# Kernel tuning notes

Hardware: AMD Instinct MI355X
Metric: run time of the kernel (lower is better)

The kernel has to match this reference:

```python
import jax, jax.numpy as jnp
import numpy as np

EPS = 1e-5

def _lrelu(x):
    return jnp.where(x >= 0, x, 0.2 * x)

def _bn(x, g, b):
    # train-mode BatchNorm2d over (B, N, k) per channel (channel-last layout)
    m = x.mean((0, 1, 2), keepdims=True)
    v = x.var((0, 1, 2), keepdims=True)  # biased variance, as torch uses for normalization
    return (x - m) * jax.lax.rsqrt(v + EPS) * g + b

def _knn(pos, k):
    # pos: (B, 3, N); negative squared euclidean distance, top-k = k nearest (incl. self)
    inner = -2.0 * jnp.einsum('bcn,bcm->bnm', pos, pos)
    xx = jnp.sum(pos * pos, axis=1)  # (B, N)
    pd = -xx[:, :, None] - inner - xx[:, None, :]  # (B, N, N)
    return jax.lax.top_k(pd, k)[1]  # (B, N, k) int32

def _edge(xt, idx):
    # xt: (B, N, C), idx: (B, N, k) -> (B, N, k, 2C) = [neighbor - center, center]
    nb = jax.vmap(lambda f, i: f[i])(xt, idx)  # (B, N, k, C) gather
    ctr = jnp.broadcast_to(xt[:, :, None, :], nb.shape)
    return jnp.concatenate([nb - ctr, ctr], axis=-1)

def _conv_bn_lrelu(h, W, g, b):
    # 1x1 conv as einsum on channel-last (B, N, k, Cin) -> (B, N, k, Cout)
    return _lrelu(_bn(jnp.einsum('bnkc,oc->bnko', h, W), g, b))

def _forward(x, k, W1, g1, b1, W2, g2, b2, W3, g3, b3, W4, g4, b4, W5, g5, b5, W9a, b9a, W9b, b9b):
    xt = x.transpose(0, 2, 1)  # (B, N, 67)
    idx = _knn(x[:, -3:, :], k)  # knn on xyz coords (dim9=True)
    h = _conv_bn_lrelu(_edge(xt, idx), W1, g1, b1)
    h = _conv_bn_lrelu(h, W2, g2, b2)
    x1 = h.max(axis=2)  # (B, N, 64) max over k neighbors
    h = _conv_bn_lrelu(_edge(x1, idx), W3, g3, b3)
    h = _conv_bn_lrelu(h, W4, g4, b4)
    x2 = h.max(axis=2)
    x3 = _conv_bn_lrelu(_edge(x2, idx), W5, g5, b5).max(axis=2)
    f = jnp.concatenate([x1, x2, x3], axis=-1)  # (B, N, 192)
    h = jax.nn.relu(jnp.einsum('bnc,oc->bno', f, W9a) + b9a)
    out = jnp.einsum('bnc,oc->bno', h, W9b) + b9b  # (B, N, 16)
    return out.transpose(0, 2, 1)  # (B, 16, N) to match torch layout

def setup_inputs() -> dict:
    key = jax.random.key(0)
    ks = jax.random.split(key, 8)
    B, C, N, K = 1, 67, 8192, 20
    s = 0.1
    return {
        'x': jax.random.normal(ks[0], (B, C, N), jnp.float32),
        'k': K,
        'W1': jax.random.normal(ks[1], (64, 134), jnp.float32) * s,
        'g1': jnp.ones((64,), jnp.float32), 'b1': jnp.zeros((64,), jnp.float32),
        'W2': jax.random.normal(ks[2], (64, 64), jnp.float32) * s,
        'g2': jnp.ones((64,), jnp.float32), 'b2': jnp.zeros((64,), jnp.float32),
        'W3': jax.random.normal(ks[3], (64, 128), jnp.float32) * s,
        'g3': jnp.ones((64,), jnp.float32), 'b3': jnp.zeros((64,), jnp.float32),
        'W4': jax.random.normal(ks[4], (64, 64), jnp.float32) * s,
        'g4': jnp.ones((64,), jnp.float32), 'b4': jnp.zeros((64,), jnp.float32),
        'W5': jax.random.normal(ks[5], (64, 128), jnp.float32) * s,
        'g5': jnp.ones((64,), jnp.float32), 'b5': jnp.zeros((64,), jnp.float32),
        'W9a': jax.random.normal(ks[6], (128, 192), jnp.float32) * s,
        'b9a': jnp.zeros((128,), jnp.float32),
        'W9b': jax.random.normal(ks[7], (16, 128), jnp.float32) * s,
        'b9b': jnp.zeros((16,), jnp.float32),
    }

def reference(x, k, W1, g1, b1, W2, g2, b2, W3, g3, b3, W4, g4, b4, W5, g5, b5, W9a, b9a, W9b, b9b):
    return _forward(x, k, W1, g1, b1, W2, g2, b2, W3, g3, b3, W4, g4, b4, W5, g5, b5, W9a, b9a, W9b, b9b)
```

## Files before the change

### kernel.cpp

```cpp
#include <hip/hip_runtime.h>

#define NPTS 8192
#define KNN  20
#define NREP 64
#define THSUB 2048
#define FCAP 256

__device__ __forceinline__ float pair_dist4(float qx, float qy, float qz, float xxn, float4 c) {
    float dot = fmaf(qz, c.z, fmaf(qy, c.y, qx * c.x));
    return fmaf(2.f, dot, -xxn) - c.w;
}
__device__ __forceinline__ float self_sq(float dx, float dy, float dz) {
    return fmaf(dz, dz, fmaf(dy, dy, dx * dx));
}
__device__ __forceinline__ float lrelu(float v) { return (v >= 0.f) ? v : 0.2f * v; }

__device__ __forceinline__ void compute_affine(const float* __restrict__ gs,
                                               const float* __restrict__ g,
                                               const float* __restrict__ b,
                                               float* saff, int tid) {
    if (tid < 64) {
        float s = 0.f, ss = 0.f;
        for (int r = 0; r < NREP; ++r) { s += gs[r * 128 + tid]; ss += gs[r * 128 + 64 + tid]; }
        const float invM = 1.f / (float)(NPTS * KNN);
        float mean = s * invM;
        float var = ss * invM - mean * mean;
        float sc = g[tid] * rsqrtf(var + 1e-5f);
        saff[tid] = sc;
        saff[64 + tid] = b[tid] - mean * sc;
    }
}

__global__ __launch_bounds__(256) void prep_kernel(const float* __restrict__ x,
                                                   const float* __restrict__ W1,
                                                   const float* __restrict__ W3,
                                                   const float* __restrict__ W5,
                                                   const float* __restrict__ W9a,
                                                   const float* __restrict__ W9b,
                                                   float4* __restrict__ pk,
                                                   float* __restrict__ Wt1,
                                                   float* __restrict__ Wt3,
                                                   float* __restrict__ Wt5,
                                                   float* __restrict__ W9at,
                                                   float* __restrict__ W9bt,
                                                   float* __restrict__ gsAll) {
    int gid = blockIdx.x * 256 + threadIdx.x;
    if (gid < NPTS) {
        float dx = x[64 * NPTS + gid], dy = x[65 * NPTS + gid], dz = x[66 * NPTS + gid];
        pk[gid] = make_float4(dx, dy, dz, self_sq(dx, dy, dz));
        return;
    }
    gid -= NPTS;
    if (gid < 67 * 128) {
        int c = gid >> 7, o = gid & 127;
        Wt1[gid] = (o < 64) ? W1[o * 134 + c] : W1[(o - 64) * 134 + 67 + c];
        return;
    }
    gid -= 67 * 128;
    if (gid < 64 * 128) {
        int c = gid >> 7, o = gid & 127;
        Wt3[gid] = (o < 64) ? W3[o * 128 + c] : W3[(o - 64) * 128 + 64 + c];
        return;
    }
    gid -= 64 * 128;
    if (gid < 64 * 128) {
        int c = gid >> 7, o = gid & 127;
        Wt5[gid] = (o < 64) ? W5[o * 128 + c] : W5[(o - 64) * 128 + 64 + c];
        return;
    }
    gid -= 64 * 128;
    if (gid < 192 * 128) {
        int c = gid >> 7, j = gid & 127;
        W9at[gid] = W9a[j * 192 + c];
        return;
    }
    gid -= 192 * 128;
    if (gid < 128 * 16) {
        int c = gid >> 4, j = gid & 15;
        W9bt[gid] = W9b[j * 128 + c];
        return;
    }
    gid -= 128 * 16;
    if (gid < 5 * NREP * 128) gsAll[gid] = 0.f;
}

__global__ __launch_bounds__(256) void knn_theta_proj(const float4* __restrict__ pk,
                                                      float* __restrict__ theta,
                                                      const float* __restrict__ X,
                                                      const float* __restrict__ Wt1,
                                                      float* __restrict__ P) {
    __shared__ float4 cpt[THSUB];
    int tid = threadIdx.x;
    if (blockIdx.x >= 512) {
        int bb = blockIdx.x - 512;
        int o = tid & 127, h = tid >> 7;
        int n0 = bb * 8 + h * 4;
        float acc[4] = {0.f, 0.f, 0.f, 0.f};
        for (int c = 0; c < 67; ++c) {
            float w = Wt1[c * 128 + o];
#pragma unroll
            for (int i = 0; i < 4; ++i) acc[i] = fmaf(X[(n0 + i) + c * NPTS], w, acc[i]);
        }
#pragma unroll
        for (int i = 0; i < 4; ++i) P[(n0 + i) * 128 + o] = acc[i];
        return;
    }
    int wid = tid >> 6, lane = tid & 63;
    int qbase = blockIdx.x * 16 + wid * 4;
    for (int i = tid; i < THSUB; i += 256) cpt[i] = pk[i];
    float qx[4], qy[4], qz[4], xxn[4], mv[4];
#pragma unroll
    for (int qi = 0; qi < 4; ++qi) {
        float4 qp = pk[qbase + qi];
        qx[qi] = qp.x; qy[qi] = qp.y; qz[qi] = qp.z; xxn[qi] = qp.w;
        mv[qi] = -INFINITY;
    }
    __syncthreads();
    for (int t = 0; t < THSUB / 64; ++t) {
        float4 c = cpt[t * 64 + lane];
#pragma unroll
        for (int qi = 0; qi < 4; ++qi)
            mv[qi] = fmaxf(mv[qi], pair_dist4(qx[qi], qy[qi], qz[qi], xxn[qi], c));
    }
#pragma unroll 1
    for (int qi = 0; qi < 4; ++qi) {
        float sel = mv[qi];
        float th = -INFINITY;
        for (int r = 0; r < KNN; ++r) {
            float v = sel;
#pragma unroll
            for (int m = 32; m >= 1; m >>= 1) v = fmaxf(v, __shfl_xor(v, m));
            th = v;
            unsigned long long bm = __ballot(sel == v);
            if (lane == __ffsll(bm) - 1) sel = -INFINITY;
        }
        if (lane == 0) theta[qbase + qi] = th - 1e-3f;
    }
}

__global__ __launch_bounds__(256) void knn_fsel(const float4* __restrict__ pk,
                                                const float* __restrict__ theta,
                                                int* __restrict__ idx_out,
                                                const float* __restrict__ P,
                                                float* __restrict__ gs) {
    __shared__ float4 cpt[1024];
    __shared__ int bufi[4][FCAP];
    int tid = threadIdx.x, wid = tid >> 6, lane = tid & 63;
    int q = blockIdx.x * 4 + wid;
    float4 qp = pk[q];
    float th = theta[q];
    int wcnt = 0;
    unsigned long long below = (1ull << lane) - 1ull;

    for (int ch = 0; ch < 8; ++ch) {
        __syncthreads();
        for (int i = tid; i < 1024; i += 256) cpt[i] = pk[ch * 1024 + i];
        __syncthreads();
        for (int t = 0; t < 16; ++t) {
            int gi = ch * 1024 + t * 64 + lane;
            float4 c = cpt[t * 64 + lane];
            float d = pair_dist4(qp.x, qp.y, qp.z, qp.w, c);
            bool p = (d >= th);
            unsigned long long mk = __ballot(p);
            if (p) {
                int pos = wcnt + (int)__popcll(mk & below);
                if (pos < FCAP) bufi[wid][pos] = gi;
            }
            wcnt += (int)__popcll(mk);
        }
    }

    int mi_keep = 0;
    if (wcnt <= FCAP) {
        float sv[4]; int si[4];
#pragma unroll
        for (int r = 0; r < 4; ++r) {
            int j = r * 64 + lane;
            bool ok = j < wcnt;
            int sidx = ok ? bufi[wid][j] : 0;
            float dv = pair_dist4(qp.x, qp.y, qp.z, qp.w, pk[sidx]);
            sv[r] = ok ? dv : -INFINITY;
            si[r] = ok ? sidx : 0x7fffffff;
        }
        for (int r = 0; r < KNN; ++r) {
            float lv = -INFINITY; int li = 0x7fffffff; int ls = -1;
#pragma unroll
            for (int s3 = 0; s3 < 4; ++s3) {
                bool g = (sv[s3] > lv) || (sv[s3] == lv && si[s3] < li);
                if (g) { lv = sv[s3]; li = si[s3]; ls = s3; }
            }
            float wv = lv; int wi = li;
#pragma unroll
            for (int m = 32; m >= 1; m >>= 1) {
                float ov = __shfl_xor(wv, m); int oi = __shfl_xor(wi, m);
                if (ov > wv || (ov == wv && oi < wi)) { wv = ov; wi = oi; }
            }
            if (lv == wv && li == wi) {
#pragma unroll
                for (int s3 = 0; s3 < 4; ++s3)
                    if (s3 == ls) { sv[s3] = -INFINITY; si[s3] = 0x7fffffff; }
            }
            if (lane == 0) idx_out[q * KNN + r] = wi;
            if (lane == r) mi_keep = wi;
        }
    } else {
        float pv = INFINITY; int pi = -1;
        for (int r = 0; r < KNN; ++r) {
            float bv = -INFINITY; int bi = 0x7fffffff;
            for (int t = 0; t < NPTS / 64; ++t) {
                int i = t * 64 + lane;
                float d = pair_dist4(qp.x, qp.y, qp.z, qp.w, pk[i]);
                bool adm = (d < pv) || (d == pv && i > pi);
                if (adm && (d > bv || (d == bv && i < bi))) { bv = d; bi = i; }
            }
            float wv = bv; int wi = bi;
#pragma unroll
            for (int m = 32; m >= 1; m >>= 1) {
                float ov = __shfl_xor(wv, m); int oi = __shfl_xor(wi, m);
                if (ov > wv || (ov == wv && oi < wi)) { wv = ov; wi = oi; }
            }
            if (lane == 0) idx_out[q * KNN + r] = wi;
            if (lane == r) mi_keep = wi;
            pv = wv; pi = wi;
        }
    }
    float An = P[q * 128 + lane];
    float Bn = P[q * 128 + 64 + lane];
    float base = Bn - An;
    float sum = 0.f, ss = 0.f;
#pragma unroll
    for (int kk = 0; kk < KNN; ++kk) {
        int m = __shfl(mi_keep, kk);
        float z = P[(size_t)m * 128 + lane] + base;
        sum += z;
        ss = fmaf(z, z, ss);
    }
    float* gg = gs + (blockIdx.x & (NREP - 1)) * 128;
    atomicAdd(gg + lane, sum);
    atomicAdd(gg + 64 + lane, ss);
}

__global__ __launch_bounds__(256) void zsum_kernel(const float* __restrict__ P,
                                                   const int* __restrict__ idx,
                                                   float* __restrict__ gs) {
    int tid = threadIdx.x;
    int o = tid & 63;
    float sum = 0.f, sumsq = 0.f;
    int n0 = blockIdx.x * 4;
#pragma unroll
    for (int ni = 0; ni < 4; ++ni) {
        int n = n0 + ni;
        float An = P[n * 128 + o];
        float Bn = P[n * 128 + 64 + o];
        float base = Bn - An;
#pragma unroll
        for (int kk2 = 0; kk2 < 5; ++kk2) {
            int kk = (tid >> 6) + kk2 * 4;
            int m = idx[n * KNN + kk];
            float z = P[m * 128 + o] + base;
            sum += z;
            sumsq = fmaf(z, z, sumsq);
        }
    }
    __shared__ float s1[256], s2[256];
    s1[tid] = sum; s2[tid] = sumsq;
    __syncthreads();
    if (tid < 64) {
        float a = s1[tid] + s1[tid + 64] + s1[tid + 128] + s1[tid + 192];
        float b = s2[tid] + s2[tid + 64] + s2[tid + 128] + s2[tid + 192];
        float* g = gs + (blockIdx.x & (NREP - 1)) * 128;
        atomicAdd(g + tid, a);
        atomicAdd(g + 64 + tid, b);
    }
}

__global__ __launch_bounds__(256) void conv_gemm_kernel(const float* __restrict__ P,
                                                        const int* __restrict__ idx,
                                                        const float* __restrict__ gsIn,
                                                        const float* __restrict__ gIn,
                                                        const float* __restrict__ bIn,
                                                        const float* __restrict__ W,
                                                        float* __restrict__ gsOut,
                                                        float* __restrict__ Mx,
                                                        float* __restrict__ Mn) {
    __shared__ float As[80][68];
    __shared__ float Ws[64][68];
    __shared__ float saff[128];
    int tid = threadIdx.x;
    int r0 = blockIdx.x * 80;

    compute_affine(gsIn, gIn, bIn, saff, tid);
    for (int i2 = tid; i2 < 1024; i2 += 256) {
        int rr = i2 >> 4, c4 = (i2 & 15) * 4;
        *(float4*)&Ws[rr][c4] = *(const float4*)&W[rr * 64 + c4];
    }
    __syncthreads();

#pragma unroll 5
    for (int i2 = tid; i2 < 1280; i2 += 256) {
        int rr = i2 >> 4, c4 = (i2 & 15) * 4;
        int grow = r0 + rr;
        int n = grow / 20;
        int m = idx[grow];
        float4 zn = *(const float4*)&P[(size_t)m * 128 + c4];
        float4 an = *(const float4*)&P[(size_t)n * 128 + c4];
        float4 bn = *(const float4*)&P[(size_t)n * 128 + 64 + c4];
        float4 ov; float z;
        z = zn.x + (bn.x - an.x); ov.x = lrelu(fmaf(z, saff[c4 + 0], saff[64 + c4 + 0]));
        z = zn.y + (bn.y - an.y); ov.y = lrelu(fmaf(z, saff[c4 + 1], saff[64 + c4 + 1]));
        z = zn.z + (bn.z - an.z); ov.z = lrelu(fmaf(z, saff[c4 + 2], saff[64 + c4 + 2]));
        z = zn.w + (bn.w - an.w); ov.w = lrelu(fmaf(z, saff[c4 + 3], saff[64 + c4 + 3]));
        *(float4*)&As[rr][c4] = ov;
    }
    __syncthreads();

    int ty = tid >> 4, tx = tid & 15;
    float acc[5][4];
#pragma unroll
    for (int i = 0; i < 5; ++i)
#pragma unroll
        for (int j = 0; j < 4; ++j) acc[i][j] = 0.f;

    for (int c4 = 0; c4 < 64; c4 += 4) {
        float4 a4[5], w4[4];
#pragma unroll
        for (int i = 0; i < 5; ++i) a4[i] = *(const float4*)&As[ty + 16 * i][c4];
#pragma unroll
        for (int j = 0; j < 4; ++j) w4[j] = *(const float4*)&Ws[tx + 16 * j][c4];
#pragma unroll
        for (int i = 0; i < 5; ++i)
#pragma unroll
            for (int j = 0; j < 4; ++j) {
                acc[i][j] = fmaf(a4[i].x, w4[j].x, acc[i][j]);
                acc[i][j] = fmaf(a4[i].y, w4[j].y, acc[i][j]);
                acc[i][j] = fmaf(a4[i].z, w4[j].z, acc[i][j]);
                acc[i][j] = fmaf(a4[i].w, w4[j].w, acc[i][j]);
            }
    }
    __syncthreads();

#pragma unroll
    for (int i = 0; i < 5; ++i)
#pragma unroll
        for (int j = 0; j < 4; ++j) As[ty + 16 * i][tx + 16 * j] = acc[i][j];
    __syncthreads();

    int a = tid >> 6, o = tid & 63;
    float mxv = -INFINITY, mnv = INFINITY, s = 0.f, ss = 0.f;
#pragma unroll
    for (int r = 0; r < 20; ++r) {
        float v = As[20 * a + r][o];
        mxv = fmaxf(mxv, v); mnv = fminf(mnv, v);
        s += v; ss = fmaf(v, v, ss);
    }
    int n = blockIdx.x * 4 + a;
    Mx[n * 64 + o] = mxv;
    Mn[n * 64 + o] = mnv;
    float* sred = &Ws[0][0];
    float* ssred = sred + 256;
    sred[a * 64 + o] = s;
    ssred[a * 64 + o] = ss;
    __syncthreads();
    if (tid < 64) {
        float ts = sred[tid] + sred[64 + tid] + sred[128 + tid] + sred[192 + tid];
        float tss = ssred[tid] + ssred[64 + tid] + ssred[128 + tid] + ssred[192 + tid];
        float* gg = gsOut + (blockIdx.x & (NREP - 1)) * 128;
        atomicAdd(gg + tid, ts);
        atomicAdd(gg + 64 + tid, tss);
    }
}

__global__ __launch_bounds__(256) void pool_proj_kernel(const float* __restrict__ Mx,
                                                        const float* __restrict__ Mn,
                                                        const float* __restrict__ gsIn,
                                                        const float* __restrict__ g,
                                                        const float* __restrict__ b,
                                                        const float* __restrict__ Wt,
                                                        float* __restrict__ Xout,
                                                        float* __restrict__ Pout) {
    __shared__ float saff[128];
    __shared__ float xs[4][64];
    int tid = threadIdx.x;
    compute_affine(gsIn, g, b, saff, tid);
    __syncthreads();
    int n0 = blockIdx.x * 4;
    int pp = tid >> 6, o = tid & 63;
    float sc = saff[o], sh = saff[64 + o];
    float v = (sc >= 0.f) ? Mx[(n0 + pp) * 64 + o] : Mn[(n0 + pp) * 64 + o];
    float xv = lrelu(fmaf(v, sc, sh));
    Xout[(n0 + pp) * 64 + o] = xv;
    xs[pp][o] = xv;
    __syncthreads();
    int o2 = tid & 127, h = tid >> 7;
    int p0 = h * 2, p1 = h * 2 + 1;
    float a0 = 0.f, a1 = 0.f;
    for (int c = 0; c < 64; ++c) {
        float w = Wt[c * 128 + o2];
        a0 = fmaf(xs[p0][c], w, a0);
        a1 = fmaf(xs[p1][c], w, a1);
    }
    Pout[(n0 + p0) * 128 + o2] = a0;
    Pout[(n0 + p1) * 128 + o2] = a1;
}

__global__ __launch_bounds__(256) void zpool_kernel(const float* __restrict__ P,
                                                    const int* __restrict__ idx,
                                                    const float* __restrict__ gsIn,
                                                    const float* __restrict__ g,
                                                    const float* __restrict__ b,
                                                    float* __restrict__ Xout) {
    __shared__ float saff[128];
    int tid = threadIdx.x;
    compute_affine(gsIn, g, b, saff, tid);
    __syncthreads();
    int gid = blockIdx.x * 256 + tid;
    int n = gid >> 6, o = gid & 63;
    float An = P[n * 128 + o];
    float Bn = P[n * 128 + 64 + o];
    float base = Bn - An;
    float mxz = -INFINITY, mnz = INFINITY;
#pragma unroll
    for (int kk = 0; kk < KNN; ++kk) {
        int m = idx[n * KNN + kk];
        float z = P[m * 128 + o] + base;
        mxz = fmaxf(mxz, z); mnz = fminf(mnz, z);
    }
    float sc = saff[o], sh = saff[64 + o];
    float v = (sc >= 0.f) ? mxz : mnz;
    Xout[gid] = lrelu(fmaf(v, sc, sh));
}

__global__ __launch_bounds__(128) void mlp_kernel(const float* __restrict__ x1,
                                                  const float* __restrict__ x2,
                                                  const float* __restrict__ x3,
                                                  const float* __restrict__ W9at,
                                                  const float* __restrict__ b9a,
                                                  const float* __restrict__ W9bt,
                                                  const float* __restrict__ b9b,
                                                  float* __restrict__ out) {
    __shared__ float hs[8][128];
    int tid = threadIdx.x;
    int j = tid;
    int n0 = blockIdx.x * 8;
    float acc[8];
    float bj = b9a[j];
#pragma unroll
    for (int p = 0; p < 8; ++p) acc[p] = bj;
    for (int c = 0; c < 64; ++c) {
        float w = W9at[c * 128 + j];
#pragma unroll
        for (int p = 0; p < 8; ++p) acc[p] = fmaf(x1[(n0 + p) * 64 + c], w, acc[p]);
    }
    for (int c = 0; c < 64; ++c) {
        float w = W9at[(64 + c) * 128 + j];
#pragma unroll
        for (int p = 0; p < 8; ++p) acc[p] = fmaf(x2[(n0 + p) * 64 + c], w, acc[p]);
    }
    for (int c = 0; c < 64; ++c) {
        float w = W9at[(128 + c) * 128 + j];
#pragma unroll
        for (int p = 0; p < 8; ++p) acc[p] = fmaf(x3[(n0 + p) * 64 + c], w, acc[p]);
    }
#pragma unroll
    for (int p = 0; p < 8; ++p) hs[p][j] = fmaxf(acc[p], 0.f);
    __syncthreads();
    int p2 = tid >> 4, j2 = tid & 15;
    float a = b9b[j2];
    for (int c = 0; c < 128; ++c) a = fmaf(hs[p2][c], W9bt[c * 16 + j2], a);
    out[j2 * NPTS + n0 + p2] = a;
}

extern "C" void kernel_launch(void* const* d_in, const int* in_sizes, int n_in,
                              void* d_out, int out_size, void* d_ws, size_t ws_size,
                              hipStream_t stream) {
    const float* x   = (const float*)d_in[0];
    const float* W1  = (const float*)d_in[2];
    const float* g1  = (const float*)d_in[3];
    const float* b1  = (const float*)d_in[4];
    const float* W2  = (const float*)d_in[5];
    const float* g2  = (const float*)d_in[6];
    const float* b2  = (const float*)d_in[7];
    const float* W3  = (const float*)d_in[8];
    const float* g3  = (const float*)d_in[9];
    const float* b3  = (const float*)d_in[10];
    const float* W4  = (const float*)d_in[11];
    const float* g4  = (const float*)d_in[12];
    const float* b4  = (const float*)d_in[13];
    const float* W5  = (const float*)d_in[14];
    const float* g5  = (const float*)d_in[15];
    const float* b5  = (const float*)d_in[16];
    const float* W9a = (const float*)d_in[17];
    const float* b9a = (const float*)d_in[18];
    const float* W9b = (const float*)d_in[19];
    const float* b9b = (const float*)d_in[20];
    float* out = (float*)d_out;

    char* ws = (char*)d_ws;
    int*    idx    = (int*)(ws + 0);
    float4* pk     = (float4*)(ws + 655360);
    float*  P      = (float*)(ws + 786432);
    float*  Mx     = (float*)(ws + 4980736);
    float*  Mn     = (float*)(ws + 7077888);
    float*  gsAll  = (float*)(ws + 9175040);
    float*  x1b    = (float*)(ws + 9338880);
    float*  x2b    = (float*)(ws + 11436032);
    float*  x3b    = (float*)(ws + 13533184);
    float*  Wt1    = (float*)(ws + 15630336);
    float*  Wt3    = (float*)(ws + 15664640);
    float*  Wt5    = (float*)(ws + 15697408);
    float*  W9at   = (float*)(ws + 15730176);
    float*  W9bt   = (float*)(ws + 15828480);
    float*  theta  = (float*)(ws + 15836672);
    (void)ws_size; (void)in_sizes; (void)n_in; (void)out_size;

    float* gs1 = gsAll;
    float* gs2 = gsAll + 1 * NREP * 128;
    float* gs3 = gsAll + 2 * NREP * 128;
    float* gs4 = gsAll + 3 * NREP * 128;
    float* gs5 = gsAll + 4 * NREP * 128;

    prep_kernel<<<394, 256, 0, stream>>>(x, W1, W3, W5, W9a, W9b, pk, Wt1, Wt3, Wt5, W9at, W9bt, gsAll);
    knn_theta_proj<<<1536, 256, 0, stream>>>(pk, theta, x, Wt1, P);
    knn_fsel<<<NPTS / 4, 256, 0, stream>>>(pk, theta, idx, P, gs1);

    conv_gemm_kernel<<<NPTS * KNN / 80, 256, 0, stream>>>(P, idx, gs1, g1, b1, W2, gs2, Mx, Mn);
    pool_proj_kernel<<<NPTS / 4, 256, 0, stream>>>(Mx, Mn, gs2, g2, b2, Wt3, x1b, P);

    zsum_kernel<<<NPTS / 4, 256, 0, stream>>>(P, idx, gs3);
    conv_gemm_kernel<<<NPTS * KNN / 80, 256, 0, stream>>>(P, idx, gs3, g3, b3, W4, gs4, Mx, Mn);
    pool_proj_kernel<<<NPTS / 4, 256, 0, stream>>>(Mx, Mn, gs4, g4, b4, Wt5, x2b, P);

    zsum_kernel<<<NPTS / 4, 256, 0, stream>>>(P, idx, gs5);
    zpool_kernel<<<NPTS * 64 / 256, 256, 0, stream>>>(P, idx, gs5, g5, b5, x3b);

    mlp_kernel<<<NPTS / 8, 128, 0, stream>>>(x1b, x2b, x3b, W9at, b9a, W9bt, b9b, out);
}
```

Baseline: 220.7 us.

## Fuse KNN threshold computation into selection kernel and fold W1 projection into prep

Removes the separate knn_theta_proj kernel. Each query's threshold is now computed inside knn_fsel over the first 2048 points, one query per wave instead of four. The first-layer projection moves into the prep kernel and reads W1 directly, without a transposed copy. This saves a kernel launch and the theta round trip through global memory, plus an added early skip when the ballot mask is empty. In exchange each fsel block loads two extra shared tiles, and the W1 reads in the projection are now strided rather than coalesced.

```diff
diff --git a/kernel.cpp b/kernel.cpp
--- a/kernel.cpp
+++ b/kernel.cpp
@@ -3,7 +3,6 @@
 #define NPTS 8192
 #define KNN  20
 #define NREP 64
-#define THSUB 2048
 #define FCAP 256
 
 __device__ __forceinline__ float pair_dist4(float qx, float qy, float qz, float xxn, float4 c) {
@@ -31,32 +30,42 @@
     }
 }
 
-__global__ __launch_bounds__(256) void prep_kernel(const float* __restrict__ x,
-                                                   const float* __restrict__ W1,
-                                                   const float* __restrict__ W3,
-                                                   const float* __restrict__ W5,
-                                                   const float* __restrict__ W9a,
-                                                   const float* __restrict__ W9b,
-                                                   float4* __restrict__ pk,
-                                                   float* __restrict__ Wt1,
-                                                   float* __restrict__ Wt3,
-                                                   float* __restrict__ Wt5,
-                                                   float* __restrict__ W9at,
-                                                   float* __restrict__ W9bt,
-                                                   float* __restrict__ gsAll) {
-    int gid = blockIdx.x * 256 + threadIdx.x;
+__global__ __launch_bounds__(256) void prep_proj_kernel(const float* __restrict__ x,
+                                                        const float* __restrict__ W1,
+                                                        const float* __restrict__ W3,
+                                                        const float* __restrict__ W5,
+                                                        const float* __restrict__ W9a,
+                                                        const float* __restrict__ W9b,
+                                                        float4* __restrict__ pk,
+                                                        float* __restrict__ Wt3,
+                                                        float* __restrict__ Wt5,
+                                                        float* __restrict__ W9at,
+                                                        float* __restrict__ W9bt,
+                                                        float* __restrict__ gsAll,
+                                                        float* __restrict__ P) {
+    int tid = threadIdx.x;
+    if (blockIdx.x >= 360) {
+        int bb = blockIdx.x - 360;
+        int o = tid & 127, h = tid >> 7;
+        int n0 = bb * 8 + h * 4;
+        float acc[4] = {0.f, 0.f, 0.f, 0.f};
+        const float* wrow = (o < 64) ? (W1 + o * 134) : (W1 + (o - 64) * 134 + 67);
+        for (int c = 0; c < 67; ++c) {
+            float w = wrow[c];
+#pragma unroll
+            for (int i = 0; i < 4; ++i) acc[i] = fmaf(x[(n0 + i) + c * NPTS], w, acc[i]);
+        }
+#pragma unroll
+        for (int i = 0; i < 4; ++i) P[(n0 + i) * 128 + o] = acc[i];
+        return;
+    }
+    int gid = blockIdx.x * 256 + tid;
     if (gid < NPTS) {
         float dx = x[64 * NPTS + gid], dy = x[65 * NPTS + gid], dz = x[66 * NPTS + gid];
         pk[gid] = make_float4(dx, dy, dz, self_sq(dx, dy, dz));
         return;
     }
     gid -= NPTS;
-    if (gid < 67 * 128) {
-        int c = gid >> 7, o = gid & 127;
-        Wt1[gid] = (o < 64) ? W1[o * 134 + c] : W1[(o - 64) * 134 + 67 + c];
-        return;
-    }
-    gid -= 67 * 128;
     if (gid < 64 * 128) {
         int c = gid >> 7, o = gid & 127;
         Wt3[gid] = (o < 64) ? W3[o * 128 + c] : W3[(o - 64) * 128 + 64 + c];
@@ -84,62 +93,7 @@
     if (gid < 5 * NREP * 128) gsAll[gid] = 0.f;
 }
 
-__global__ __launch_bounds__(256) void knn_theta_proj(const float4* __restrict__ pk,
-                                                      float* __restrict__ theta,
-                                                      const float* __restrict__ X,
-                                                      const float* __restrict__ Wt1,
-                                                      float* __restrict__ P) {
-    __shared__ float4 cpt[THSUB];
-    int tid = threadIdx.x;
-    if (blockIdx.x >= 512) {
-        int bb = blockIdx.x - 512;
-        int o = tid & 127, h = tid >> 7;
-        int n0 = bb * 8 + h * 4;
-        float acc[4] = {0.f, 0.f, 0.f, 0.f};
-        for (int c = 0; c < 67; ++c) {
-            float w = Wt1[c * 128 + o];
-#pragma unroll
-            for (int i = 0; i < 4; ++i) acc[i] = fmaf(X[(n0 + i) + c * NPTS], w, acc[i]);
-        }
-#pragma unroll
-        for (int i = 0; i < 4; ++i) P[(n0 + i) * 128 + o] = acc[i];
-        return;
-    }
-    int wid = tid >> 6, lane = tid & 63;
-    int qbase = blockIdx.x * 16 + wid * 4;
-    for (int i = tid; i < THSUB; i += 256) cpt[i] = pk[i];
-    float qx[4], qy[4], qz[4], xxn[4], mv[4];
-#pragma unroll
-    for (int qi = 0; qi < 4; ++qi) {
-        float4 qp = pk[qbase + qi];
-        qx[qi] = qp.x; qy[qi] = qp.y; qz[qi] = qp.z; xxn[qi] = qp.w;
-        mv[qi] = -INFINITY;
-    }
-    __syncthreads();
-    for (int t = 0; t < THSUB / 64; ++t) {
-        float4 c = cpt[t * 64 + lane];
-#pragma unroll
-        for (int qi = 0; qi < 4; ++qi)
-            mv[qi] = fmaxf(mv[qi], pair_dist4(qx[qi], qy[qi], qz[qi], xxn[qi], c));
-    }
-#pragma unroll 1
-    for (int qi = 0; qi < 4; ++qi) {
-        float sel = mv[qi];
-        float th = -INFINITY;
-        for (int r = 0; r < KNN; ++r) {
-            float v = sel;
-#pragma unroll
-            for (int m = 32; m >= 1; m >>= 1) v = fmaxf(v, __shfl_xor(v, m));
-            th = v;
-            unsigned long long bm = __ballot(sel == v);
-            if (lane == __ffsll(bm) - 1) sel = -INFINITY;
-        }
-        if (lane == 0) theta[qbase + qi] = th - 1e-3f;
-    }
-}
-
 __global__ __launch_bounds__(256) void knn_fsel(const float4* __restrict__ pk,
-                                                const float* __restrict__ theta,
                                                 int* __restrict__ idx_out,
                                                 const float* __restrict__ P,
                                                 float* __restrict__ gs) {
@@ -148,10 +102,28 @@
     int tid = threadIdx.x, wid = tid >> 6, lane = tid & 63;
     int q = blockIdx.x * 4 + wid;
     float4 qp = pk[q];
-    float th = theta[q];
+    unsigned long long below = (1ull << lane) - 1ull;
+
+    float mv = -INFINITY;
+    for (int ch = 0; ch < 2; ++ch) {
+        __syncthreads();
+        for (int i = tid; i < 1024; i += 256) cpt[i] = pk[ch * 1024 + i];
+        __syncthreads();
+        for (int t = 0; t < 16; ++t)
+            mv = fmaxf(mv, pair_dist4(qp.x, qp.y, qp.z, qp.w, cpt[t * 64 + lane]));
+    }
+    float sel = mv, th = -INFINITY;
+    for (int r = 0; r < KNN; ++r) {
+        float v = sel;
+#pragma unroll
+        for (int m = 32; m >= 1; m >>= 1) v = fmaxf(v, __shfl_xor(v, m));
+        th = v;
+        unsigned long long bm = __ballot(sel == v);
+        if (lane == __ffsll(bm) - 1) sel = -INFINITY;
+    }
+    th -= 1e-3f;
+
     int wcnt = 0;
-    unsigned long long below = (1ull << lane) - 1ull;
-
     for (int ch = 0; ch < 8; ++ch) {
         __syncthreads();
         for (int i = tid; i < 1024; i += 256) cpt[i] = pk[ch * 1024 + i];
@@ -162,11 +134,13 @@
             float d = pair_dist4(qp.x, qp.y, qp.z, qp.w, c);
             bool p = (d >= th);
             unsigned long long mk = __ballot(p);
-            if (p) {
-                int pos = wcnt + (int)__popcll(mk & below);
-                if (pos < FCAP) bufi[wid][pos] = gi;
-            }
-            wcnt += (int)__popcll(mk);
+            if (mk) {
+                if (p) {
+                    int pos = wcnt + (int)__popcll(mk & below);
+                    if (pos < FCAP) bufi[wid][pos] = gi;
+                }
+                wcnt += (int)__popcll(mk);
+            }
         }
     }
 
@@ -505,12 +479,10 @@
     float*  x1b    = (float*)(ws + 9338880);
     float*  x2b    = (float*)(ws + 11436032);
     float*  x3b    = (float*)(ws + 13533184);
-    float*  Wt1    = (float*)(ws + 15630336);
     float*  Wt3    = (float*)(ws + 15664640);
     float*  Wt5    = (float*)(ws + 15697408);
     float*  W9at   = (float*)(ws + 15730176);
     float*  W9bt   = (float*)(ws + 15828480);
-    float*  theta  = (float*)(ws + 15836672);
     (void)ws_size; (void)in_sizes; (void)n_in; (void)out_size;
 
     float* gs1 = gsAll;
@@ -519,9 +491,8 @@
     float* gs4 = gsAll + 3 * NREP * 128;
     float* gs5 = gsAll + 4 * NREP * 128;
 
-    prep_kernel<<<394, 256, 0, stream>>>(x, W1, W3, W5, W9a, W9b, pk, Wt1, Wt3, Wt5, W9at, W9bt, gsAll);
-    knn_theta_proj<<<1536, 256, 0, stream>>>(pk, theta, x, Wt1, P);
-    knn_fsel<<<NPTS / 4, 256, 0, stream>>>(pk, theta, idx, P, gs1);
+    prep_proj_kernel<<<1384, 256, 0, stream>>>(x, W1, W3, W5, W9a, W9b, pk, Wt3, Wt5, W9at, W9bt, gsAll, P);
+    knn_fsel<<<NPTS / 4, 256, 0, stream>>>(pk, idx, P, gs1);
 
     conv_gemm_kernel<<<NPTS * KNN / 80, 256, 0, stream>>>(P, idx, gs1, g1, b1, W2, gs2, Mx, Mn);
     pool_proj_kernel<<<NPTS / 4, 256, 0, stream>>>(Mx, Mn, gs2, g2, b2, Wt3, x1b, P);
```

Result: slower. 240.9 us (+9.2%).
